# Kernel optimization log

Hardware: AMD Instinct MI355X
Metric: run time of the kernel (lower is better)

The kernel has to match this reference:

```python
import jax, jax.numpy as jnp
import numpy as np

S, D_MODEL, H, D_K, D_V = 2048, 1024, 16, 64, 64


def setup_inputs() -> dict:
    key = jax.random.key(0)
    ks = jax.random.split(key, 10)
    sd = 0.02
    return {
        "embeddings": jax.random.normal(ks[0], (S, D_MODEL), dtype=jnp.float32),
        # per-head projection weights (torch Linear: y = x @ W.T + b; here stored as [h, d_in, d_out])
        "Wq": jax.random.normal(ks[1], (H, D_MODEL, D_K), dtype=jnp.float32) * sd,
        "bq": jax.random.normal(ks[2], (H, D_K), dtype=jnp.float32) * sd,
        "Wk": jax.random.normal(ks[3], (H, D_MODEL, D_K), dtype=jnp.float32) * sd,
        "bk": jax.random.normal(ks[4], (H, D_K), dtype=jnp.float32) * sd,
        "Wv": jax.random.normal(ks[5], (H, D_MODEL, D_V), dtype=jnp.float32) * sd,
        "bv": jax.random.normal(ks[6], (H, D_V), dtype=jnp.float32) * sd,
        "Wo": jax.random.normal(ks[7], (H * D_V, D_MODEL), dtype=jnp.float32) * sd,
        "bo": jax.random.normal(ks[8], (D_MODEL,), dtype=jnp.float32) * sd,
    }


def reference(embeddings, Wq, bq, Wk, bk, Wv, bv, Wo, bo):
    # Batched equivalent of the per-head Python loop of ScaledDotProductAttention layers.
    # q,k: [h, s, d_k]; v: [h, s, d_v]
    q = jnp.einsum('sd,hdk->hsk', embeddings, Wq) + bq[:, None, :]
    k = jnp.einsum('sd,hdk->hsk', embeddings, Wk) + bk[:, None, :]
    v = jnp.einsum('sd,hdv->hsv', embeddings, Wv) + bv[:, None, :]
    scale = jnp.asarray(1.0 / np.sqrt(q.shape[-1]), q.dtype)
    scores = jnp.einsum('hsk,htk->hst', q, k) * scale  # [h, s, s]
    attn = jax.nn.softmax(scores, axis=-1)
    heads = jnp.einsum('hst,htv->hsv', attn, v)  # [h, s, d_v]
    # torch.cat(results, dim=1): head outputs concatenated along feature dim -> [s, h*d_v]
    concat = jnp.transpose(heads, (1, 0, 2)).reshape(embeddings.shape[0], -1)
    return concat @ Wo + bo
```

## Files before the change

### kernel.cpp

```cpp
#include <hip/hip_runtime.h>
#include <hip/hip_bf16.h>

typedef unsigned short u16;
typedef __attribute__((ext_vector_type(8))) short bf16x8;
typedef __attribute__((ext_vector_type(4))) float f32x4;
typedef __attribute__((ext_vector_type(16))) float f32x16;

#define S_LEN 2048
#define NH 16

__device__ __forceinline__ u16 f2bf(float x) {
  union { float f; unsigned u; } v; v.f = x;
  unsigned r = v.u + 0x7fffu + ((v.u >> 16) & 1u);
  return (u16)(r >> 16);
}

__device__ __forceinline__ unsigned cvtpk_bf16(float lo, float hi) {
  unsigned w;
  asm("v_cvt_pk_bf16_f32 %0, %1, %2" : "=v"(w) : "v"(lo), "v"(hi));
  return w;
}

__device__ __forceinline__ void plswap(unsigned& a, unsigned& b) {
  asm volatile("v_permlane32_swap_b32 %0, %1" : "+v"(a), "+v"(b));
}

__device__ __forceinline__ float fexp2(float x) {
#if __has_builtin(__builtin_amdgcn_exp2f)
  return __builtin_amdgcn_exp2f(x);
#else
  float y;
  asm volatile("v_exp_f32 %0, %1\n\ts_nop 0" : "=v"(y) : "v"(x));
  return y;
#endif
}

__device__ __forceinline__ void async16(const void* g, void* l) {
  __builtin_amdgcn_global_load_lds(
      (const __attribute__((address_space(1))) unsigned int*)g,
      (__attribute__((address_space(3))) unsigned int*)l, 16, 0, 0);
}

__device__ __forceinline__ f32x4 mfma16(bf16x8 a, bf16x8 b, f32x4 c) {
  return __builtin_amdgcn_mfma_f32_16x16x32_bf16(a, b, c, 0, 0, 0);
}
__device__ __forceinline__ f32x16 mfma32(bf16x8 a, bf16x8 b, f32x16 c) {
  return __builtin_amdgcn_mfma_f32_32x32x16_bf16(a, b, c, 0, 0, 0);
}

#define QSCALE (0.125f * 1.44269504089f)

__global__ __launch_bounds__(256) void convert_kernel(
    const float* __restrict__ emb, const float* __restrict__ Wq,
    const float* __restrict__ Wk, const float* __restrict__ Wv,
    const float* __restrict__ bq, const float* __restrict__ bk,
    const float* __restrict__ bv, const float* __restrict__ Wo,
    u16* __restrict__ emb_bf, u16* __restrict__ wqkv_t,
    u16* __restrict__ wo_t, float* __restrict__ bqkv) {
  __shared__ float lds[64][65];
  const int b = blockIdx.x, tid = threadIdx.x;
  if (b < 2048) {
    int i = b * 1024 + tid * 4;
    float4 v = *(const float4*)(emb + i);
    ushort4 o = {f2bf(v.x), f2bf(v.y), f2bf(v.z), f2bf(v.w)};
    *(ushort4*)(emb_bf + i) = o;
    return;
  }
  if (b < 2816) {
    int tt = b - 2048;
    int kind = tt >> 8;
    int rem = tt & 255;
    int h = rem >> 4, k0 = (rem & 15) << 6;
    const float* W = (kind == 0) ? Wq : ((kind == 1) ? Wk : Wv);
    const float* src = W + ((size_t)h * 1024 + k0) * 64;
#pragma unroll
    for (int rr = 0; rr < 4; ++rr) {
      int k = rr * 16 + (tid >> 4);
      int d4 = (tid & 15) << 2;
      float4 v = *(const float4*)(src + (size_t)k * 64 + d4);
      lds[k][d4] = v.x; lds[k][d4 + 1] = v.y;
      lds[k][d4 + 2] = v.z; lds[k][d4 + 3] = v.w;
    }
    __syncthreads();
    float scale = (kind == 0) ? QSCALE : 1.f;
#pragma unroll
    for (int p = 0; p < 2; ++p) {
      int d = p * 32 + (tid >> 3);
      int kb = (tid & 7) << 3;
      bf16x8 o;
#pragma unroll
      for (int j = 0; j < 8; ++j) o[j] = (short)f2bf(lds[kb + j][d] * scale);
      *(bf16x8*)(wqkv_t + (size_t)(kind * 1024 + h * 64 + d) * 1024 + k0 + kb) = o;
    }
    return;
  }
  if (b < 3072) {
    int tt = b - 2816;
    int k0 = (tt >> 4) << 6, n0 = (tt & 15) << 6;
#pragma unroll
    for (int rr = 0; rr < 4; ++rr) {
      int k = rr * 16 + (tid >> 4);
      int n4 = (tid & 15) << 2;
      float4 v = *(const float4*)(Wo + (size_t)(k0 + k) * 1024 + n0 + n4);
      lds[k][n4] = v.x; lds[k][n4 + 1] = v.y;
      lds[k][n4 + 2] = v.z; lds[k][n4 + 3] = v.w;
    }
    __syncthreads();
#pragma unroll
    for (int p = 0; p < 2; ++p) {
      int nrel = p * 32 + (tid >> 3);
      int kb = (tid & 7) << 3;
      bf16x8 o;
#pragma unroll
      for (int j = 0; j < 8; ++j) o[j] = (short)f2bf(lds[kb + j][nrel]);
      *(bf16x8*)(wo_t + (size_t)(n0 + nrel) * 1024 + k0 + kb) = o;
    }
    return;
  }
  for (int i = tid; i < 3072; i += 256) {
    int kind = i >> 10, hd = i & 1023;
    const float* bb = (kind == 0) ? bq : ((kind == 1) ? bk : bv);
    float v = bb[hd];
    bqkv[i] = (kind == 0) ? v * QSCALE : v;
  }
}

template <int WM, int WN, int FM, int FN, int BK, bool OUT_BF16, bool SPLIT>
__global__ __launch_bounds__(WM * WN * 64) void gemm_kernel(
    const u16* __restrict__ A, const u16* __restrict__ BT,
    const float* __restrict__ bias, void* __restrict__ Cout,
    u16* __restrict__ kp, u16* __restrict__ vp, int M, int N, int K) {
  constexpr int BM = WM * FM * 16, BN = WN * FN * 16, T = WM * WN * 64;
  constexpr int RB = BK * 2;
  __shared__ u16 lds[2][(BM + BN) * BK];
  const int tid = threadIdx.x;
  const int lane = tid & 63, wave = tid >> 6;
  const int wr = wave / WN, wc = wave % WN;
  const int m0 = blockIdx.x * BM, n0 = blockIdx.y * BN;
  const int r = lane & 15, g = lane >> 4;
  const f32x4 fzero = {0.f, 0.f, 0.f, 0.f};
  f32x4 acc[FM][FN];
#pragma unroll
  for (int i = 0; i < FM; ++i)
#pragma unroll
    for (int j = 0; j < FN; ++j) acc[i][j] = fzero;

  constexpr int LA = (BM * RB) / (T * 16);
  constexpr int LB = (BN * RB) / (T * 16);

  auto stage = [&](int kt, int buf) {
    int k0 = kt * BK;
#pragma unroll
    for (int i = 0; i < LA; ++i) {
      int flat = i * T * 16 + tid * 16;
      int row = flat / RB, colb = flat % RB;
      async16((const char*)A + ((size_t)(m0 + row) * K + k0) * 2 + colb,
              (char*)lds[buf] + i * T * 16 + wave * 1024);
    }
#pragma unroll
    for (int i = 0; i < LB; ++i) {
      int flat = i * T * 16 + tid * 16;
      int row = flat / RB, colb = flat % RB;
      async16((const char*)BT + ((size_t)(n0 + row) * K + k0) * 2 + colb,
              (char*)lds[buf] + BM * RB + i * T * 16 + wave * 1024);
    }
  };

  stage(0, 0);
  asm volatile("s_waitcnt vmcnt(0)" ::: "memory");
  __syncthreads();

  const int NT = K / BK;
  for (int kt = 0; kt < NT; ++kt) {
    int cur = kt & 1;
    if (kt + 1 < NT) stage(kt + 1, cur ^ 1);
    const u16* Al = lds[cur];
    const u16* Bl = Al + BM * BK;
#pragma unroll
    for (int kk = 0; kk < BK / 32; ++kk) {
      bf16x8 af[FM], bfr[FN];
#pragma unroll
      for (int i = 0; i < FM; ++i)
        af[i] = *(const bf16x8*)&Al[(wr * FM * 16 + i * 16 + r) * BK + kk * 32 + g * 8];
#pragma unroll
      for (int j = 0; j < FN; ++j)
        bfr[j] = *(const bf16x8*)&Bl[(wc * FN * 16 + j * 16 + r) * BK + kk * 32 + g * 8];
#pragma unroll
      for (int i = 0; i < FM; ++i)
#pragma unroll
        for (int j = 0; j < FN; ++j)
          acc[i][j] = mfma16(af[i], bfr[j], acc[i][j]);
    }
    asm volatile("s_waitcnt vmcnt(0)" ::: "memory");
    __syncthreads();
  }

  if constexpr (SPLIT) {
    if (n0 >= 2048) {
      int h = (n0 - 2048) >> 6;
      u16* base = vp + (size_t)h * 131072;
#pragma unroll
      for (int i = 0; i < FM; ++i)
#pragma unroll
        for (int j = 0; j < FN; ++j) {
          int d = wc * FN * 16 + j * 16 + r;
          int t0v = m0 + wr * FM * 16 + i * 16 + g * 4;
          float bval = bias[n0 + d];
          int off = (t0v >> 6) * 4096 + ((((t0v >> 4) & 3) * 2 + (d >> 5))) * 512 +
                    ((d & 31) * 2 + ((t0v >> 3) & 1)) * 8 + (t0v & 7);
          ushort4 o = {f2bf(acc[i][j][0] + bval), f2bf(acc[i][j][1] + bval),
                       f2bf(acc[i][j][2] + bval), f2bf(acc[i][j][3] + bval)};
          *(ushort4*)(base + off) = o;
        }
      return;
    }
    if (n0 >= 1024) {
      int h = (n0 - 1024) >> 6;
      u16* base = kp + (size_t)h * 131072;
#pragma unroll
      for (int i = 0; i < FM; ++i)
#pragma unroll
        for (int j = 0; j < FN; ++j) {
          int d = wc * FN * 16 + j * 16 + r;
          float bval = bias[n0 + d];
#pragma unroll
          for (int e = 0; e < 4; ++e) {
            int t = m0 + wr * FM * 16 + i * 16 + g * 4 + e;
            int off = (t >> 5) * 2048 + (d >> 4) * 512 +
                      ((t & 31) * 2 + ((d >> 3) & 1)) * 8 + (d & 7);
            base[off] = f2bf(acc[i][j][e] + bval);
          }
        }
      return;
    }
#pragma unroll
    for (int i = 0; i < FM; ++i)
#pragma unroll
      for (int j = 0; j < FN; ++j)
#pragma unroll
        for (int e = 0; e < 4; ++e) {
          int row = m0 + wr * FM * 16 + i * 16 + g * 4 + e;
          int col = n0 + wc * FN * 16 + j * 16 + r;
          ((u16*)Cout)[(size_t)row * 1024 + col] = f2bf(acc[i][j][e] + bias[col]);
        }
    return;
  }

#pragma unroll
  for (int i = 0; i < FM; ++i)
#pragma unroll
    for (int j = 0; j < FN; ++j)
#pragma unroll
      for (int e = 0; e < 4; ++e) {
        int row = m0 + wr * FM * 16 + i * 16 + g * 4 + e;
        int col = n0 + wc * FN * 16 + j * 16 + r;
        float v = acc[i][j][e] + bias[col];
        if constexpr (OUT_BF16)
          ((u16*)Cout)[(size_t)row * N + col] = f2bf(v);
        else
          ((float*)Cout)[(size_t)row * N + col] = v;
      }
}

__global__ __launch_bounds__(256, 1) void attn_kernel(const u16* __restrict__ qbuf,
                                                      const u16* __restrict__ kp,
                                                      const u16* __restrict__ vp,
                                                      u16* __restrict__ concat) {
  const int tid = threadIdx.x, lane = tid & 63, wave = tid >> 6;
  const int swz = (blockIdx.x & 7) * 32 + (blockIdx.x >> 3);
  const int h = swz >> 4, qg = swz & 15;
  const int q0w = qg * 128 + wave * 32;
  const int l31 = lane & 31, hi5 = lane >> 5;
  const char* kb = (const char*)kp + (size_t)h * 262144;
  const char* vb = (const char*)vp + (size_t)h * 262144;
  const int loff = (l31 * 2 + hi5) * 16;

  bf16x8 qf[4];
#pragma unroll
  for (int ds = 0; ds < 4; ++ds)
    qf[ds] = *(const bf16x8*)&qbuf[(size_t)(q0w + l31) * 1024 + h * 64 + ds * 16 + hi5 * 8];

  f32x16 acc0 = {}, acc1 = {};
  float rs = 0.f;

  bf16x8 kA[8], kB[8];
#pragma unroll
  for (int i = 0; i < 8; ++i) kA[i] = *(const bf16x8*)(kb + i * 1024 + loff);

  auto stepf = [&](int t, bf16x8(&kc)[8], bf16x8(&kn)[8]) {
    bf16x8 vF[8];
    const char* vbase = vb + (size_t)t * 8192;
#pragma unroll
    for (int i = 0; i < 8; ++i) vF[i] = *(const bf16x8*)(vbase + i * 1024 + loff);
    const char* knb = kb + (size_t)(t + 1) * 8192;
#pragma unroll
    for (int i = 0; i < 8; ++i) kn[i] = *(const bf16x8*)(knb + i * 1024 + loff);

    f32x16 sv0 = {}, sv1 = {};
    __builtin_amdgcn_s_setprio(1);
#pragma unroll
    for (int ds = 0; ds < 4; ++ds) {
      sv0 = mfma32(kc[ds], qf[ds], sv0);
      sv1 = mfma32(kc[4 + ds], qf[ds], sv1);
    }
    __builtin_amdgcn_s_setprio(0);

    bf16x8 pa[4];
#pragma unroll
    for (int s = 0; s < 2; ++s) {
      float e[16];
#pragma unroll
      for (int c = 0; c < 16; ++c) {
        e[c] = fexp2(s == 0 ? sv0[c] : sv1[c]);
        rs += e[c];
      }
      unsigned u0 = cvtpk_bf16(e[0], e[1]), v0 = cvtpk_bf16(e[2], e[3]);
      unsigned w0 = cvtpk_bf16(e[4], e[5]), z0 = cvtpk_bf16(e[6], e[7]);
      plswap(u0, w0);
      plswap(v0, z0);
      uint4 pk0 = {u0, v0, w0, z0};
      pa[2 * s] = *(bf16x8*)&pk0;
      unsigned u1 = cvtpk_bf16(e[8], e[9]), v1 = cvtpk_bf16(e[10], e[11]);
      unsigned w1 = cvtpk_bf16(e[12], e[13]), z1 = cvtpk_bf16(e[14], e[15]);
      plswap(u1, w1);
      plswap(v1, z1);
      uint4 pk1 = {u1, v1, w1, z1};
      pa[2 * s + 1] = *(bf16x8*)&pk1;
    }

    __builtin_amdgcn_s_setprio(1);
#pragma unroll
    for (int tsl = 0; tsl < 4; ++tsl) {
      acc0 = mfma32(pa[tsl], vF[tsl * 2 + 0], acc0);
      acc1 = mfma32(pa[tsl], vF[tsl * 2 + 1], acc1);
    }
    __builtin_amdgcn_s_setprio(0);
  };

  for (int t = 0; t < 32; t += 2) {
    stepf(t, kA, kB);
    stepf(t + 1, kB, kA);
  }

  rs += __shfl_xor(rs, 32, 64);

#pragma unroll
  for (int c = 0; c < 16; ++c) {
    int q = (c & 3) + 8 * (c >> 2) + 4 * hi5;
    float dn = __shfl(rs, q, 64);
    float inv = 1.f / dn;
    size_t rowb = (size_t)(q0w + q) * 1024 + h * 64;
    concat[rowb + l31] = f2bf(acc0[c] * inv);
    concat[rowb + 32 + l31] = f2bf(acc1[c] * inv);
  }
}

extern "C" void kernel_launch(void* const* d_in, const int* in_sizes, int n_in,
                              void* d_out, int out_size, void* d_ws,
                              size_t ws_size, hipStream_t stream) {
  (void)in_sizes; (void)n_in; (void)out_size; (void)ws_size;
  const float* emb = (const float*)d_in[0];
  const float* Wq = (const float*)d_in[1];
  const float* bq = (const float*)d_in[2];
  const float* Wk = (const float*)d_in[3];
  const float* bk = (const float*)d_in[4];
  const float* Wv = (const float*)d_in[5];
  const float* bv = (const float*)d_in[6];
  const float* Wo = (const float*)d_in[7];
  const float* bo = (const float*)d_in[8];

  char* ws = (char*)d_ws;
  u16* emb_bf  = (u16*)(ws + 0);
  u16* wqkv_t  = (u16*)(ws + 4194304);
  u16* wo_t    = (u16*)(ws + 10485760);
  float* bqkv  = (float*)(ws + 12582912);
  u16* qbuf    = (u16*)(ws + 12595200);
  u16* kpack   = (u16*)(ws + 16789504);
  u16* vpack   = (u16*)(ws + 20983808);
  u16* concat  = (u16*)(ws + 29372416);

  convert_kernel<<<3073, 256, 0, stream>>>(emb, Wq, Wk, Wv, bq, bk, bv, Wo,
                                           emb_bf, wqkv_t, wo_t, bqkv);
  gemm_kernel<2, 2, 4, 2, 64, true, true><<<dim3(16, 48), 256, 0, stream>>>(
      emb_bf, wqkv_t, bqkv, qbuf, kpack, vpack, 2048, 3072, 1024);
  attn_kernel<<<256, 256, 0, stream>>>(qbuf, kpack, vpack, concat);
  gemm_kernel<2, 2, 2, 2, 64, false, false><<<dim3(32, 16), 256, 0, stream>>>(
      concat, wo_t, bo, d_out, nullptr, nullptr, 2048, 1024, 1024);
}
```

Before: 73.20 us.

## Split KV range across waves in attention and combine partials via LDS

Each attention block now handles 64 queries with two wave pairs that each process half of the key/value sequence. The second wave of each pair writes its partial output and row sums to shared memory, and the first wave merges them and normalizes. The grid doubles to 512 blocks and launch bounds allow two blocks per CU, to raise occupancy and latency hiding. The cost is an LDS reduction, a block barrier, and a tighter register budget per thread.

```diff
diff --git a/kernel.cpp b/kernel.cpp
--- a/kernel.cpp
+++ b/kernel.cpp
@@ -262,14 +262,18 @@
       }
 }
 
-__global__ __launch_bounds__(256, 1) void attn_kernel(const u16* __restrict__ qbuf,
+__global__ __launch_bounds__(256, 2) void attn_kernel(const u16* __restrict__ qbuf,
                                                       const u16* __restrict__ kp,
                                                       const u16* __restrict__ vp,
                                                       u16* __restrict__ concat) {
+  __shared__ float Ox[2][32][64];
+  __shared__ float Lx[2][32];
   const int tid = threadIdx.x, lane = tid & 63, wave = tid >> 6;
-  const int swz = (blockIdx.x & 7) * 32 + (blockIdx.x >> 3);
-  const int h = swz >> 4, qg = swz & 15;
-  const int q0w = qg * 128 + wave * 32;
+  const int qs = wave >> 1, kvw = wave & 1;
+  const int slot = blockIdx.x >> 3;
+  const int h = (blockIdx.x & 7) * 2 + (slot >> 5);
+  const int qg = slot & 31;
+  const int q0w = qg * 64 + qs * 32;
   const int l31 = lane & 31, hi5 = lane >> 5;
   const char* kb = (const char*)kp + (size_t)h * 262144;
   const char* vb = (const char*)vp + (size_t)h * 262144;
@@ -283,9 +287,11 @@
   f32x16 acc0 = {}, acc1 = {};
   float rs = 0.f;
 
+  const int tbeg = kvw * 16, tend = tbeg + 16;
   bf16x8 kA[8], kB[8];
 #pragma unroll
-  for (int i = 0; i < 8; ++i) kA[i] = *(const bf16x8*)(kb + i * 1024 + loff);
+  for (int i = 0; i < 8; ++i)
+    kA[i] = *(const bf16x8*)(kb + (size_t)tbeg * 8192 + i * 1024 + loff);
 
   auto stepf = [&](int t, bf16x8(&kc)[8], bf16x8(&kn)[8]) {
     bf16x8 vF[8];
@@ -337,21 +343,33 @@
     __builtin_amdgcn_s_setprio(0);
   };
 
-  for (int t = 0; t < 32; t += 2) {
+  for (int t = tbeg; t < tend; t += 2) {
     stepf(t, kA, kB);
     stepf(t + 1, kB, kA);
   }
 
   rs += __shfl_xor(rs, 32, 64);
 
-#pragma unroll
-  for (int c = 0; c < 16; ++c) {
-    int q = (c & 3) + 8 * (c >> 2) + 4 * hi5;
-    float dn = __shfl(rs, q, 64);
-    float inv = 1.f / dn;
-    size_t rowb = (size_t)(q0w + q) * 1024 + h * 64;
-    concat[rowb + l31] = f2bf(acc0[c] * inv);
-    concat[rowb + 32 + l31] = f2bf(acc1[c] * inv);
+  if (kvw == 1) {
+#pragma unroll
+    for (int c = 0; c < 16; ++c) {
+      int q = (c & 3) + 8 * (c >> 2) + 4 * hi5;
+      Ox[qs][q][l31] = acc0[c];
+      Ox[qs][q][32 + l31] = acc1[c];
+    }
+    if (hi5 == 0) Lx[qs][l31] = rs;
+  }
+  __syncthreads();
+  if (kvw == 0) {
+#pragma unroll
+    for (int c = 0; c < 16; ++c) {
+      int q = (c & 3) + 8 * (c >> 2) + 4 * hi5;
+      float dn = __shfl(rs, q, 64) + Lx[qs][q];
+      float inv = 1.f / dn;
+      size_t rowb = (size_t)(q0w + q) * 1024 + h * 64;
+      concat[rowb + l31] = f2bf((acc0[c] + Ox[qs][q][l31]) * inv);
+      concat[rowb + 32 + l31] = f2bf((acc1[c] + Ox[qs][q][32 + l31]) * inv);
+    }
   }
 }
 
@@ -383,7 +401,7 @@
                                            emb_bf, wqkv_t, wo_t, bqkv);
   gemm_kernel<2, 2, 4, 2, 64, true, true><<<dim3(16, 48), 256, 0, stream>>>(
       emb_bf, wqkv_t, bqkv, qbuf, kpack, vpack, 2048, 3072, 1024);
-  attn_kernel<<<256, 256, 0, stream>>>(qbuf, kpack, vpack, concat);
+  attn_kernel<<<512, 256, 0, stream>>>(qbuf, kpack, vpack, concat);
   gemm_kernel<2, 2, 2, 2, 64, false, false><<<dim3(32, 16), 256, 0, stream>>>(
       concat, wo_t, bo, d_out, nullptr, nullptr, 2048, 1024, 1024);
 }
```

Measured after the change: 74.86 us. 1.02x slower.
